# Performance work log

Measured on AMD Instinct MI355X. Metric: run time of the kernel, lower is better.

## Reference

```python
import jax, jax.numpy as jnp
import numpy as np

N_SPECIES = 16
D_HIDDEN = 32
TOP_K = 4


def setup_inputs() -> dict:
    key = jax.random.key(0)
    ks = jax.random.split(key, 9)
    s = 0.1
    x = jax.random.uniform(ks[0], (16, 4096, N_SPECIES), jnp.float32, 0.01, 2.0)
    w_in = jax.random.normal(ks[1], (D_HIDDEN, 2), jnp.float32) * s        # Linear(2, d) weight
    species_emb = jax.random.normal(ks[2], (N_SPECIES, D_HIDDEN), jnp.float32) * 0.1
    gat_w0 = jax.random.normal(ks[3], (D_HIDDEN, D_HIDDEN), jnp.float32) * s
    gat_a0 = jax.random.normal(ks[4], (2 * D_HIDDEN,), jnp.float32) * s    # Linear(2d, 1) weight
    gat_w1 = jax.random.normal(ks[5], (D_HIDDEN, D_HIDDEN), jnp.float32) * s
    gat_a1 = jax.random.normal(ks[6], (2 * D_HIDDEN,), jnp.float32) * s
    w_out = jax.random.normal(ks[7], (1, D_HIDDEN), jnp.float32) * s
    b_out = jnp.zeros((1,), jnp.float32)
    r_intrinsic = jnp.zeros((N_SPECIES,), jnp.float32)
    return dict(x=x, w_in=w_in, species_emb=species_emb,
                gat_w0=gat_w0, gat_a0=gat_a0, gat_w1=gat_w1, gat_a1=gat_a1,
                w_out=w_out, b_out=b_out, r_intrinsic=r_intrinsic)


def _gat_layer(h, w, a, top_k):
    # h: (M, N, d). torch Linear: h @ w.T
    d = h.shape[-1]
    hw = h @ w.T                                     # (M, N, d)
    # scores[b,n,m] = a . cat(hw[b,n], hw[b,m]) = s_i[b,n] + s_j[b,m]
    # (avoids materializing the (M,N,N,2d) pair tensor; identical math)
    s_i = hw @ a[:d]                                 # (M, N)
    s_j = hw @ a[d:]                                 # (M, N)
    scores = s_i[:, :, None] + s_j[:, None, :]       # (M, N, N)
    n = scores.shape[-1]
    k_eff = min(top_k, n)
    _, idx = jax.lax.top_k(scores, k_eff)            # (M, N, k)
    keep = jax.nn.one_hot(idx, n, dtype=jnp.bool_).any(axis=-2)  # (M, N, N)
    masked = jnp.where(keep, scores, -jnp.inf)       # non-topk -> -inf (== scatter of topk vals)
    attn = jax.nn.softmax(masked, axis=-1)
    return jnp.einsum('bnm,bmd->bnd', attn, hw)


def reference(x, w_in, species_emb, gat_w0, gat_a0, gat_w1, gat_a1, w_out, b_out, r_intrinsic):
    B, T, N = x.shape
    safe = jnp.clip(x, 1e-6, None)
    feats = jnp.stack([x, jnp.log(safe)], axis=-1)           # (B, T, N, 2)
    h = feats @ w_in.T + species_emb                         # (B, T, N, d)
    h = h.reshape(B * T, N, -1)
    for w, a in ((gat_w0, gat_a0), (gat_w1, gat_a1)):
        h = h + _gat_layer(h, w, a, TOP_K)
    out = (h @ w_out.T + b_out)[..., 0]                      # (B*T, N)
    return out.reshape(B, T, N) + r_intrinsic
```

## Files before the change

kernel.cpp:

```cpp
#include <hip/hip_runtime.h>

#define QP_XOR1 0xB1
#define QP_XOR2 0x4E

template<int CTRL>
__device__ __forceinline__ float dpp_f(float v) {
    return __builtin_bit_cast(float,
        __builtin_amdgcn_update_dpp(0, __builtin_bit_cast(int, v), CTRL, 0xF, 0xF, true));
}
__device__ __forceinline__ float qsum(float v) {
    v += dpp_f<QP_XOR1>(v);
    v += dpp_f<QP_XOR2>(v);
    return v;
}

template<int CTRL>
__device__ __forceinline__ void merge4(float& t0, float& t1, float& t2, float& t3) {
    const float p0 = dpp_f<CTRL>(t0), p1 = dpp_f<CTRL>(t1), p2 = dpp_f<CTRL>(t2), p3 = dpp_f<CTRL>(t3);
    const float c0 = fmaxf(t0, p3), c1 = fmaxf(t1, p2), c2 = fmaxf(t2, p1), c3 = fmaxf(t3, p0);
    const float d0 = fmaxf(c0, c2), d2 = fminf(c0, c2);
    const float d1 = fmaxf(c1, c3), d3 = fminf(c1, c3);
    t0 = fmaxf(d0, d1); t1 = fminf(d0, d1);
    t2 = fmaxf(d2, d3); t3 = fminf(d2, d3);
}

__device__ __forceinline__ void gat4(const float s[4], const float xv[4], const float lx[4],
                                     const float4 ce, float& X, float& Lo, float& A) {
    const float a0 = fmaxf(s[0], s[1]), a1 = fminf(s[0], s[1]);
    const float a2 = fmaxf(s[2], s[3]), a3 = fminf(s[2], s[3]);
    const float b0 = fmaxf(a0, a2), b2 = fminf(a0, a2);
    const float b1 = fmaxf(a1, a3), b3 = fminf(a1, a3);
    float t0 = b0, t1 = fmaxf(b1, b2), t2 = fminf(b1, b2), t3 = b3;
    merge4<QP_XOR1>(t0, t1, t2, t3);
    merge4<QP_XOR2>(t0, t1, t2, t3);
    const float m = t0, tau = t3;
    const float e0 = (s[0] >= tau) ? __expf(s[0] - m) : 0.f;
    const float e1 = (s[1] >= tau) ? __expf(s[1] - m) : 0.f;
    const float e2 = (s[2] >= tau) ? __expf(s[2] - m) : 0.f;
    const float e3 = (s[3] >= tau) ? __expf(s[3] - m) : 0.f;
    const float rd = __builtin_amdgcn_rcpf(qsum((e0 + e1) + (e2 + e3)));
    X  = qsum(fmaf(e3, xv[3], fmaf(e2, xv[2], fmaf(e1, xv[1], e0 * xv[0])))) * rd;
    Lo = qsum(fmaf(e3, lx[3], fmaf(e2, lx[2], fmaf(e1, lx[1], e0 * lx[0])))) * rd;
    A  = qsum(fmaf(e3, ce.w,  fmaf(e2, ce.z,  fmaf(e1, ce.y,  e0 * ce.x)))) * rd;
}

#define U_WOUT 0
#define U_A0H  32
#define U_A1H  64
#define U_G0   96
#define U_G1   128
#define U_C0   160
#define U_C1   192
#define U_GS   224
#define LBR    256
#define LZERO  272
#define LDUMP  288
#define LCST   544
#define LDS_FLOATS 704

__device__ __forceinline__ void job32(float* L, int uoff, const float* __restrict__ vb,
                                      int vstr, int dst, int eoff) {
    float acc = 0.f;
    #pragma unroll
    for (int j = 0; j < 32; ++j) acc = fmaf(L[uoff + j], vb[j * vstr], acc);
    L[dst] = acc + L[eoff];
}

__device__ __forceinline__ void eval_graph(
    const float4 xv4, const float4 g0q, const float4 g1q,
    const float4 ce0q, const float4 ce1q, const float4 keq,
    float A0c, float B0c, float A1c, float B1c,
    float KX, float KL, float C0X, float C0L, float C1X, float C1L,
    float4& o)
{
    float xv[4] = {xv4.x, xv4.y, xv4.z, xv4.w};
    float lx[4], s0[4], s1[4];
    const float g0a[4] = {g0q.x, g0q.y, g0q.z, g0q.w};
    const float g1a[4] = {g1q.x, g1q.y, g1q.z, g1q.w};
    #pragma unroll
    for (int i = 0; i < 4; ++i) {
        lx[i] = __logf(fmaxf(xv[i], 1e-6f));
        s0[i] = fmaf(A0c, xv[i], fmaf(B0c, lx[i], g0a[i]));
        s1[i] = fmaf(A1c, xv[i], fmaf(B1c, lx[i], g1a[i]));
    }
    float X0, L0, A0v, X1, L1, A1v;
    gat4(s0, xv, lx, ce0q, X0, L0, A0v);
    gat4(s1, xv, lx, ce1q, X1, L1, A1v);
    const float base = fmaf(X0, C0X, fmaf(L0, C0L, A0v)) + fmaf(X1, C1X, fmaf(L1, C1L, A1v));
    o.x = fmaf(KX, xv[0], fmaf(KL, lx[0], keq.x + base));
    o.y = fmaf(KX, xv[1], fmaf(KL, lx[1], keq.y + base));
    o.z = fmaf(KX, xv[2], fmaf(KL, lx[2], keq.z + base));
    o.w = fmaf(KX, xv[3], fmaf(KL, lx[3], keq.w + base));
}

__global__ __launch_bounds__(256) void UltraSparseGNN_fused(
    const float* __restrict__ x,
    const float* __restrict__ w_in,
    const float* __restrict__ emb,
    const float* __restrict__ w0,
    const float* __restrict__ a0,
    const float* __restrict__ w1,
    const float* __restrict__ a1,
    const float* __restrict__ w_out,
    const float* __restrict__ b_out,
    const float* __restrict__ r_int,
    float* __restrict__ out,
    int total4, int half)
{
    __shared__ __align__(16) float L[LDS_FLOATS];
    const int tid = threadIdx.x;

    if (tid < 32)        L[U_WOUT + tid]      = w_out[tid];
    else if (tid < 64)   L[U_A0H + tid - 32]  = a0[32 + tid - 32];
    else if (tid < 96)   L[U_A1H + tid - 64]  = a1[32 + tid - 64];
    else if (tid < 112)  L[LBR + tid - 96]    = r_int[tid - 96] + b_out[0];
    else if (tid == 112) L[LZERO]             = 0.f;
    __syncthreads();

    {
        int uoff = U_WOUT, vstr = 0, dst = LDUMP + tid, eoff = LZERO;
        const float* vb = w0;
        if (tid < 32)        { vb = w0 + tid;              vstr = 32; dst = U_G0 + tid; }
        else if (tid < 64)   { vb = w1 + (tid - 32);       vstr = 32; dst = U_G1 + (tid - 32); }
        else if (tid < 96)   { uoff = U_A0H; vb = w0 + (tid - 64); vstr = 32; dst = U_C0 + (tid - 64); }
        else if (tid < 128)  { uoff = U_A1H; vb = w1 + (tid - 96); vstr = 32; dst = U_C1 + (tid - 96); }
        else if (tid < 144)  { vb = emb + (tid - 128) * 32; vstr = 1; dst = LCST + 80 + (tid - 128); eoff = LBR + (tid - 128); }
        else if (tid == 144) { vb = w_in;     vstr = 2; dst = LCST + 4; }
        else if (tid == 145) { vb = w_in + 1; vstr = 2; dst = LCST + 5; }
        job32(L, uoff, vb, vstr, dst, eoff);
    }
    __syncthreads();

    {
        int uoff = U_G1, vstr = 0, dst = LDUMP + tid, eoff = LZERO;
        const float* vb = w0;
        if (tid < 32)        { vb = w0 + tid; vstr = 32; dst = U_GS + tid; eoff = U_G0 + tid; }
        else if (tid < 48)   { uoff = U_C0; vb = emb + (tid - 32) * 32; vstr = 1; dst = LCST + 16 + (tid - 32); }
        else if (tid < 64)   { uoff = U_C1; vb = emb + (tid - 48) * 32; vstr = 1; dst = LCST + 32 + (tid - 48); }
        else if (tid < 80)   { vb = emb + (tid - 64) * 32; vstr = 1; dst = LCST + 64 + (tid - 64); }
        else if (tid == 80)  { uoff = U_C0; vb = w_in;     vstr = 2; dst = LCST + 0; }
        else if (tid == 81)  { uoff = U_C0; vb = w_in + 1; vstr = 2; dst = LCST + 1; }
        else if (tid == 82)  { uoff = U_C1; vb = w_in;     vstr = 2; dst = LCST + 2; }
        else if (tid == 83)  { uoff = U_C1; vb = w_in + 1; vstr = 2; dst = LCST + 3; }
        else if (tid == 84)  { vb = w_in;     vstr = 2; dst = LCST + 8; }
        else if (tid == 85)  { vb = w_in + 1; vstr = 2; dst = LCST + 9; }
        job32(L, uoff, vb, vstr, dst, eoff);
    }
    __syncthreads();

    {
        int vstr = 0, dst = LDUMP + tid;
        const float* vb = w0;
        if (tid < 16)        { vb = emb + tid * 32; vstr = 1; dst = LCST + 48 + tid; }
        else if (tid == 16)  { vb = w_in;     vstr = 2; dst = LCST + 6; }
        else if (tid == 17)  { vb = w_in + 1; vstr = 2; dst = LCST + 7; }
        job32(L, U_GS, vb, vstr, dst, LZERO);
    }
    __syncthreads();

    const int tA = blockIdx.x * 256 + tid;
    if (tA >= total4) return;
    const int q = tid & 3;

    const float4 scA = *reinterpret_cast<const float4*>(&L[LCST + 0]);
    const float4 scB = *reinterpret_cast<const float4*>(&L[LCST + 4]);
    const float C1X = L[LCST + 8], C1L = L[LCST + 9];
    const float4 g0q  = *reinterpret_cast<const float4*>(&L[LCST + 16 + q * 4]);
    const float4 g1q  = *reinterpret_cast<const float4*>(&L[LCST + 32 + q * 4]);
    const float4 ce0q = *reinterpret_cast<const float4*>(&L[LCST + 48 + q * 4]);
    const float4 ce1q = *reinterpret_cast<const float4*>(&L[LCST + 64 + q * 4]);
    const float4 keq  = *reinterpret_cast<const float4*>(&L[LCST + 80 + q * 4]);

    const float4 xvA = reinterpret_cast<const float4*>(x)[tA];
    const int tB = tA + half;
    const bool doB = (tB < total4);
    float4 xvB = xvA;
    if (doB) xvB = reinterpret_cast<const float4*>(x)[tB];

    float4 oA, oB;
    eval_graph(xvA, g0q, g1q, ce0q, ce1q, keq,
               scA.x, scA.y, scA.z, scA.w, scB.x, scB.y, scB.z, scB.w, C1X, C1L, oA);
    eval_graph(xvB, g0q, g1q, ce0q, ce1q, keq,
               scA.x, scA.y, scA.z, scA.w, scB.x, scB.y, scB.z, scB.w, C1X, C1L, oB);

    reinterpret_cast<float4*>(out)[tA] = oA;
    if (doB) reinterpret_cast<float4*>(out)[tB] = oB;
}

extern "C" void kernel_launch(void* const* d_in, const int* in_sizes, int n_in,
                              void* d_out, int out_size, void* d_ws, size_t ws_size,
                              hipStream_t stream) {
    const float* x     = (const float*)d_in[0];
    const float* w_in  = (const float*)d_in[1];
    const float* emb   = (const float*)d_in[2];
    const float* w0    = (const float*)d_in[3];
    const float* a0    = (const float*)d_in[4];
    const float* w1    = (const float*)d_in[5];
    const float* a1    = (const float*)d_in[6];
    const float* w_out = (const float*)d_in[7];
    const float* b_out = (const float*)d_in[8];
    const float* r_int = (const float*)d_in[9];

    const int total  = in_sizes[0];
    const int total4 = total >> 2;
    const int half   = (((total4 + 1) >> 1) + 3) & ~3;
    const int blocks = (half + 255) / 256;
    UltraSparseGNN_fused<<<blocks, 256, 0, stream>>>(
        x, w_in, emb, w0, a0, w1, a1, w_out, b_out, r_int,
        (float*)d_out, total4, half);
}
```

Measured before the change: 12.74 us.

## Stage weights in LDS, one float4 per thread, compute softmax max early

New measurement: 13.08 us. 2.7% more time.

```diff
diff --git a/kernel.cpp b/kernel.cpp
--- a/kernel.cpp
+++ b/kernel.cpp
@@ -26,6 +26,12 @@
 
 __device__ __forceinline__ void gat4(const float s[4], const float xv[4], const float lx[4],
                                      const float4 ce, float& X, float& Lo, float& A) {
+    float m = fmaxf(fmaxf(s[0], s[1]), fmaxf(s[2], s[3]));
+    m = fmaxf(m, dpp_f<QP_XOR1>(m));
+    m = fmaxf(m, dpp_f<QP_XOR2>(m));
+    float e0 = __expf(s[0] - m), e1 = __expf(s[1] - m);
+    float e2 = __expf(s[2] - m), e3 = __expf(s[3] - m);
+
     const float a0 = fmaxf(s[0], s[1]), a1 = fminf(s[0], s[1]);
     const float a2 = fmaxf(s[2], s[3]), a3 = fminf(s[2], s[3]);
     const float b0 = fmaxf(a0, a2), b2 = fminf(a0, a2);
@@ -33,64 +39,42 @@
     float t0 = b0, t1 = fmaxf(b1, b2), t2 = fminf(b1, b2), t3 = b3;
     merge4<QP_XOR1>(t0, t1, t2, t3);
     merge4<QP_XOR2>(t0, t1, t2, t3);
-    const float m = t0, tau = t3;
-    const float e0 = (s[0] >= tau) ? __expf(s[0] - m) : 0.f;
-    const float e1 = (s[1] >= tau) ? __expf(s[1] - m) : 0.f;
-    const float e2 = (s[2] >= tau) ? __expf(s[2] - m) : 0.f;
-    const float e3 = (s[3] >= tau) ? __expf(s[3] - m) : 0.f;
+    const float tau = t3;
+
+    e0 = (s[0] >= tau) ? e0 : 0.f;
+    e1 = (s[1] >= tau) ? e1 : 0.f;
+    e2 = (s[2] >= tau) ? e2 : 0.f;
+    e3 = (s[3] >= tau) ? e3 : 0.f;
+
     const float rd = __builtin_amdgcn_rcpf(qsum((e0 + e1) + (e2 + e3)));
     X  = qsum(fmaf(e3, xv[3], fmaf(e2, xv[2], fmaf(e1, xv[1], e0 * xv[0])))) * rd;
     Lo = qsum(fmaf(e3, lx[3], fmaf(e2, lx[2], fmaf(e1, lx[1], e0 * lx[0])))) * rd;
     A  = qsum(fmaf(e3, ce.w,  fmaf(e2, ce.z,  fmaf(e1, ce.y,  e0 * ce.x)))) * rd;
 }
 
-#define U_WOUT 0
-#define U_A0H  32
-#define U_A1H  64
-#define U_G0   96
-#define U_G1   128
-#define U_C0   160
-#define U_C1   192
-#define U_GS   224
-#define LBR    256
-#define LZERO  272
-#define LDUMP  288
-#define LCST   544
-#define LDS_FLOATS 704
-
-__device__ __forceinline__ void job32(float* L, int uoff, const float* __restrict__ vb,
-                                      int vstr, int dst, int eoff) {
+#define SW0   0
+#define SW1   1024
+#define SEMBT 2048
+#define SWIN  2560
+#define SWOUT 2624
+#define SA0H  2656
+#define SA1H  2688
+#define SBR   2720
+#define SZERO 2736
+#define G0    2752
+#define G1    2785
+#define C0    2818
+#define C1    2851
+#define GS    2884
+#define LDUMP 2917
+#define LCST  3176
+#define LDS_FLOATS 3272
+
+__device__ __forceinline__ void job32L(float* L, int uoff, int voff, int vstr, int dst, int eoff) {
     float acc = 0.f;
     #pragma unroll
-    for (int j = 0; j < 32; ++j) acc = fmaf(L[uoff + j], vb[j * vstr], acc);
+    for (int j = 0; j < 32; ++j) acc = fmaf(L[uoff + j], L[voff + j * vstr], acc);
     L[dst] = acc + L[eoff];
-}
-
-__device__ __forceinline__ void eval_graph(
-    const float4 xv4, const float4 g0q, const float4 g1q,
-    const float4 ce0q, const float4 ce1q, const float4 keq,
-    float A0c, float B0c, float A1c, float B1c,
-    float KX, float KL, float C0X, float C0L, float C1X, float C1L,
-    float4& o)
-{
-    float xv[4] = {xv4.x, xv4.y, xv4.z, xv4.w};
-    float lx[4], s0[4], s1[4];
-    const float g0a[4] = {g0q.x, g0q.y, g0q.z, g0q.w};
-    const float g1a[4] = {g1q.x, g1q.y, g1q.z, g1q.w};
-    #pragma unroll
-    for (int i = 0; i < 4; ++i) {
-        lx[i] = __logf(fmaxf(xv[i], 1e-6f));
-        s0[i] = fmaf(A0c, xv[i], fmaf(B0c, lx[i], g0a[i]));
-        s1[i] = fmaf(A1c, xv[i], fmaf(B1c, lx[i], g1a[i]));
-    }
-    float X0, L0, A0v, X1, L1, A1v;
-    gat4(s0, xv, lx, ce0q, X0, L0, A0v);
-    gat4(s1, xv, lx, ce1q, X1, L1, A1v);
-    const float base = fmaf(X0, C0X, fmaf(L0, C0L, A0v)) + fmaf(X1, C1X, fmaf(L1, C1L, A1v));
-    o.x = fmaf(KX, xv[0], fmaf(KL, lx[0], keq.x + base));
-    o.y = fmaf(KX, xv[1], fmaf(KL, lx[1], keq.y + base));
-    o.z = fmaf(KX, xv[2], fmaf(KL, lx[2], keq.z + base));
-    o.w = fmaf(KX, xv[3], fmaf(KL, lx[3], keq.w + base));
 }
 
 __global__ __launch_bounds__(256) void UltraSparseGNN_fused(
@@ -105,61 +89,75 @@
     const float* __restrict__ b_out,
     const float* __restrict__ r_int,
     float* __restrict__ out,
-    int total4, int half)
+    int total4)
 {
     __shared__ __align__(16) float L[LDS_FLOATS];
     const int tid = threadIdx.x;
 
-    if (tid < 32)        L[U_WOUT + tid]      = w_out[tid];
-    else if (tid < 64)   L[U_A0H + tid - 32]  = a0[32 + tid - 32];
-    else if (tid < 96)   L[U_A1H + tid - 64]  = a1[32 + tid - 64];
-    else if (tid < 112)  L[LBR + tid - 96]    = r_int[tid - 96] + b_out[0];
-    else if (tid == 112) L[LZERO]             = 0.f;
+    ((float4*)&L[SW0])[tid] = ((const float4*)w0)[tid];
+    ((float4*)&L[SW1])[tid] = ((const float4*)w1)[tid];
+    if (tid < 128) {
+        const float4 e = ((const float4*)emb)[tid];
+        const int n = tid >> 3, j = (tid & 7) * 4;
+        L[SEMBT + (j + 0) * 16 + n] = e.x;
+        L[SEMBT + (j + 1) * 16 + n] = e.y;
+        L[SEMBT + (j + 2) * 16 + n] = e.z;
+        L[SEMBT + (j + 3) * 16 + n] = e.w;
+    } else if (tid < 144) {
+        ((float4*)&L[SWIN])[tid - 128] = ((const float4*)w_in)[tid - 128];
+    } else if (tid < 152) {
+        ((float4*)&L[SWOUT])[tid - 144] = ((const float4*)w_out)[tid - 144];
+    } else if (tid < 160) {
+        ((float4*)&L[SA0H])[tid - 152] = ((const float4*)a0)[(tid - 152) + 8];
+    } else if (tid < 168) {
+        ((float4*)&L[SA1H])[tid - 160] = ((const float4*)a1)[(tid - 160) + 8];
+    } else if (tid < 184) {
+        L[SBR + tid - 168] = r_int[tid - 168] + b_out[0];
+    } else if (tid == 184) {
+        L[SZERO] = 0.f;
+    }
     __syncthreads();
 
     {
-        int uoff = U_WOUT, vstr = 0, dst = LDUMP + tid, eoff = LZERO;
-        const float* vb = w0;
-        if (tid < 32)        { vb = w0 + tid;              vstr = 32; dst = U_G0 + tid; }
-        else if (tid < 64)   { vb = w1 + (tid - 32);       vstr = 32; dst = U_G1 + (tid - 32); }
-        else if (tid < 96)   { uoff = U_A0H; vb = w0 + (tid - 64); vstr = 32; dst = U_C0 + (tid - 64); }
-        else if (tid < 128)  { uoff = U_A1H; vb = w1 + (tid - 96); vstr = 32; dst = U_C1 + (tid - 96); }
-        else if (tid < 144)  { vb = emb + (tid - 128) * 32; vstr = 1; dst = LCST + 80 + (tid - 128); eoff = LBR + (tid - 128); }
-        else if (tid == 144) { vb = w_in;     vstr = 2; dst = LCST + 4; }
-        else if (tid == 145) { vb = w_in + 1; vstr = 2; dst = LCST + 5; }
-        job32(L, uoff, vb, vstr, dst, eoff);
+        int uoff = SWOUT, voff = SWOUT, vstr = 0, dst = LDUMP + tid, eoff = SZERO;
+        if (tid < 32)        { voff = SW0 + tid;        vstr = 32; dst = G0 + tid; }
+        else if (tid < 64)   { voff = SW1 + tid - 32;   vstr = 32; dst = G1 + tid - 32; }
+        else if (tid < 96)   { uoff = SA0H; voff = SW0 + tid - 64; vstr = 32; dst = C0 + tid - 64; }
+        else if (tid < 128)  { uoff = SA1H; voff = SW1 + tid - 96; vstr = 32; dst = C1 + tid - 96; }
+        else if (tid < 144)  { voff = SEMBT + tid - 128; vstr = 16; dst = LCST + 80 + tid - 128; eoff = SBR + tid - 128; }
+        else if (tid == 144) { voff = SWIN;     vstr = 2; dst = LCST + 4; }
+        else if (tid == 145) { voff = SWIN + 1; vstr = 2; dst = LCST + 5; }
+        job32L(L, uoff, voff, vstr, dst, eoff);
     }
     __syncthreads();
 
     {
-        int uoff = U_G1, vstr = 0, dst = LDUMP + tid, eoff = LZERO;
-        const float* vb = w0;
-        if (tid < 32)        { vb = w0 + tid; vstr = 32; dst = U_GS + tid; eoff = U_G0 + tid; }
-        else if (tid < 48)   { uoff = U_C0; vb = emb + (tid - 32) * 32; vstr = 1; dst = LCST + 16 + (tid - 32); }
-        else if (tid < 64)   { uoff = U_C1; vb = emb + (tid - 48) * 32; vstr = 1; dst = LCST + 32 + (tid - 48); }
-        else if (tid < 80)   { vb = emb + (tid - 64) * 32; vstr = 1; dst = LCST + 64 + (tid - 64); }
-        else if (tid == 80)  { uoff = U_C0; vb = w_in;     vstr = 2; dst = LCST + 0; }
-        else if (tid == 81)  { uoff = U_C0; vb = w_in + 1; vstr = 2; dst = LCST + 1; }
-        else if (tid == 82)  { uoff = U_C1; vb = w_in;     vstr = 2; dst = LCST + 2; }
-        else if (tid == 83)  { uoff = U_C1; vb = w_in + 1; vstr = 2; dst = LCST + 3; }
-        else if (tid == 84)  { vb = w_in;     vstr = 2; dst = LCST + 8; }
-        else if (tid == 85)  { vb = w_in + 1; vstr = 2; dst = LCST + 9; }
-        job32(L, uoff, vb, vstr, dst, eoff);
+        int uoff = SWOUT, voff = SWOUT, vstr = 0, dst = LDUMP + tid, eoff = SZERO;
+        if (tid < 32)        { uoff = G1; voff = SW0 + tid; vstr = 32; dst = GS + tid; eoff = G0 + tid; }
+        else if (tid < 48)   { uoff = C0; voff = SEMBT + tid - 32; vstr = 16; dst = LCST + 16 + tid - 32; }
+        else if (tid < 64)   { uoff = C1; voff = SEMBT + tid - 48; vstr = 16; dst = LCST + 32 + tid - 48; }
+        else if (tid < 80)   { uoff = G1; voff = SEMBT + tid - 64; vstr = 16; dst = LCST + 64 + tid - 64; }
+        else if (tid == 80)  { uoff = C0; voff = SWIN;     vstr = 2; dst = LCST + 0; }
+        else if (tid == 81)  { uoff = C0; voff = SWIN + 1; vstr = 2; dst = LCST + 1; }
+        else if (tid == 82)  { uoff = C1; voff = SWIN;     vstr = 2; dst = LCST + 2; }
+        else if (tid == 83)  { uoff = C1; voff = SWIN + 1; vstr = 2; dst = LCST + 3; }
+        else if (tid == 84)  { uoff = G1; voff = SWIN;     vstr = 2; dst = LCST + 8; }
+        else if (tid == 85)  { uoff = G1; voff = SWIN + 1; vstr = 2; dst = LCST + 9; }
+        job32L(L, uoff, voff, vstr, dst, eoff);
     }
     __syncthreads();
 
     {
-        int vstr = 0, dst = LDUMP + tid;
-        const float* vb = w0;
-        if (tid < 16)        { vb = emb + tid * 32; vstr = 1; dst = LCST + 48 + tid; }
-        else if (tid == 16)  { vb = w_in;     vstr = 2; dst = LCST + 6; }
-        else if (tid == 17)  { vb = w_in + 1; vstr = 2; dst = LCST + 7; }
-        job32(L, U_GS, vb, vstr, dst, LZERO);
-    }
-    __syncthreads();
-
-    const int tA = blockIdx.x * 256 + tid;
-    if (tA >= total4) return;
+        int voff = SWOUT, vstr = 0, dst = LDUMP + tid;
+        if (tid < 16)        { voff = SEMBT + tid; vstr = 16; dst = LCST + 48 + tid; }
+        else if (tid == 16)  { voff = SWIN;     vstr = 2; dst = LCST + 6; }
+        else if (tid == 17)  { voff = SWIN + 1; vstr = 2; dst = LCST + 7; }
+        job32L(L, GS, voff, vstr, dst, SZERO);
+    }
+    __syncthreads();
+
+    const int idx = blockIdx.x * 256 + tid;
+    if (idx >= total4) return;
     const int q = tid & 3;
 
     const float4 scA = *reinterpret_cast<const float4*>(&L[LCST + 0]);
@@ -171,20 +169,29 @@
     const float4 ce1q = *reinterpret_cast<const float4*>(&L[LCST + 64 + q * 4]);
     const float4 keq  = *reinterpret_cast<const float4*>(&L[LCST + 80 + q * 4]);
 
-    const float4 xvA = reinterpret_cast<const float4*>(x)[tA];
-    const int tB = tA + half;
-    const bool doB = (tB < total4);
-    float4 xvB = xvA;
-    if (doB) xvB = reinterpret_cast<const float4*>(x)[tB];
-
-    float4 oA, oB;
-    eval_graph(xvA, g0q, g1q, ce0q, ce1q, keq,
-               scA.x, scA.y, scA.z, scA.w, scB.x, scB.y, scB.z, scB.w, C1X, C1L, oA);
-    eval_graph(xvB, g0q, g1q, ce0q, ce1q, keq,
-               scA.x, scA.y, scA.z, scA.w, scB.x, scB.y, scB.z, scB.w, C1X, C1L, oB);
-
-    reinterpret_cast<float4*>(out)[tA] = oA;
-    if (doB) reinterpret_cast<float4*>(out)[tB] = oB;
+    const float4 xv4 = reinterpret_cast<const float4*>(x)[idx];
+    float xv[4] = {xv4.x, xv4.y, xv4.z, xv4.w};
+    float lx[4], s0[4], s1[4];
+    const float g0a[4] = {g0q.x, g0q.y, g0q.z, g0q.w};
+    const float g1a[4] = {g1q.x, g1q.y, g1q.z, g1q.w};
+    #pragma unroll
+    for (int i = 0; i < 4; ++i) {
+        lx[i] = __logf(fmaxf(xv[i], 1e-6f));
+        s0[i] = fmaf(scA.x, xv[i], fmaf(scA.y, lx[i], g0a[i]));
+        s1[i] = fmaf(scA.z, xv[i], fmaf(scA.w, lx[i], g1a[i]));
+    }
+
+    float X0, L0, A0v, X1, L1, A1v;
+    gat4(s0, xv, lx, ce0q, X0, L0, A0v);
+    gat4(s1, xv, lx, ce1q, X1, L1, A1v);
+
+    const float base = fmaf(X0, scB.z, fmaf(L0, scB.w, A0v)) + fmaf(X1, C1X, fmaf(L1, C1L, A1v));
+    float4 o;
+    o.x = fmaf(scB.x, xv[0], fmaf(scB.y, lx[0], keq.x + base));
+    o.y = fmaf(scB.x, xv[1], fmaf(scB.y, lx[1], keq.y + base));
+    o.z = fmaf(scB.x, xv[2], fmaf(scB.y, lx[2], keq.z + base));
+    o.w = fmaf(scB.x, xv[3], fmaf(scB.y, lx[3], keq.w + base));
+    reinterpret_cast<float4*>(out)[idx] = o;
 }
 
 extern "C" void kernel_launch(void* const* d_in, const int* in_sizes, int n_in,
@@ -203,9 +210,8 @@
 
     const int total  = in_sizes[0];
     const int total4 = total >> 2;
-    const int half   = (((total4 + 1) >> 1) + 3) & ~3;
-    const int blocks = (half + 255) / 256;
+    const int blocks = (total4 + 255) / 256;
     UltraSparseGNN_fused<<<blocks, 256, 0, stream>>>(
         x, w_in, emb, w0, a0, w1, a1, w_out, b_out, r_int,
-        (float*)d_out, total4, half);
-}
+        (float*)d_out, total4);
+}
```
